# Kernel optimization log

Measured on AMD Instinct MI355X. Metric: run time of the kernel, lower is better.

Reference implementation:

```python
import jax, jax.numpy as jnp
import numpy as np

# Dim order: [N, K, C, P, Q, R, S]; memory levels: [L0_Registers, L1_Accumulator, L2_Scratchpad, L3_DRAM]
# Tensor types: 0=Input(N,C,P,Q) 1=Weight(K,C,R,S) 2=Output(N,K,P,Q)
DIM_MASK = jnp.array([[1,0,1,1,1,0,0],
                      [0,1,1,0,0,1,1],
                      [1,1,0,1,1,0,0]], dtype=bool)
# reuse dims: Input->K, Weight->N,P,Q, Output->C,R,S
REUSE_MASK = jnp.array([[0,1,0,0,0,0,0],
                        [1,0,0,1,1,0,0],
                        [0,0,1,0,0,1,1]], dtype=bool)

BYTES = 4.0
CLK_MHZ = 1000.0
DRAM_BW_GB_S = 100.0
PE_MAC_EPA_PJ = 0.56
L0_REG_EPA_PJ = 0.18
L1_BASE_EPA_PJ = 0.52
L1_COEFF_PJ_KB = 0.01
L2_BASE_EPA_PJ = 1.2
L2_COEFF_PJ_KB = 0.002
AREA_PER_PE = 0.01
AREA_PER_KB = 0.005

G = 500000  # number of (unfused) layers / fusion groups


def setup_inputs() -> dict:
    key = jax.random.key(0)
    k1, k2 = jax.random.split(key)
    temporal = 1.0 + jax.random.uniform(k1, (G, 7, 4), dtype=jnp.float32)
    spatial = 1.0 + jax.random.uniform(k2, (G, 7, 4), dtype=jnp.float32)
    return {
        "temporal_factors": temporal,
        "spatial_factors": spatial,
        "num_pes": jnp.array([256.0], dtype=jnp.float32),
        "buffer_sizes_kb": jnp.array([1.0, 64.0, 512.0], dtype=jnp.float32),  # L0, L1, L2
    }


def _masked_prod(x, mask):
    # x: [G,7,L], mask: [3,7] -> [G,3,L] product over masked dims
    return jnp.prod(jnp.where(mask[None, :, :, None], x[:, None, :, :], 1.0), axis=2)


def reference(temporal_factors, spatial_factors, num_pes, buffer_sizes_kb):
    pe = num_pes[0]
    sq = jnp.sqrt(pe)

    cumTS = jnp.cumprod(temporal_factors * spatial_factors, axis=2)  # prefix prod over levels
    cumT = jnp.cumprod(temporal_factors, axis=2)
    sufT = jnp.flip(jnp.cumprod(jnp.flip(temporal_factors, 2), 2), 2)  # suffix prod over levels

    macs = jnp.prod(cumTS[:, :, -1], axis=1)  # [G] product of full dim sizes

    fp = _masked_prod(cumTS, DIM_MASK)      # [G,3,4] data footprint up to level l
    outer = _masked_prod(sufT, DIM_MASK)    # [G,3,4] outer iterations from level l up
    ru = _masked_prod(cumT, REUSE_MASK)     # [G,3,4] reuse factor up to level l

    # interfaces (upper->lower): L3->L2, L2->L1, L1->L0
    low = jnp.array([2, 1, 0])
    up = jnp.array([3, 2, 1])
    acc = (fp[:, :, low] * (outer[:, :, up] / (ru[:, :, low] + 1e-9)) * BYTES).sum(axis=1)  # [G,3]

    # latency
    onchip_bw = 2.0 * sq * BYTES * CLK_MHZ * 1e6 / 1e9
    bw = jnp.stack([jnp.full((), DRAM_BW_GB_S), onchip_bw, onchip_bw])  # upper level bw per interface
    mem_lat = acc / (bw[None, :] * 1e9 + 1e-9)
    comp_lat = macs / (pe * CLK_MHZ * 1e6 + 1e-9)
    total_latency = jnp.maximum(comp_lat, mem_lat.max(axis=1)).sum()

    # energy (per interface, keyed by lower level: L2, L1, L0)
    epa = jnp.stack([
        L2_BASE_EPA_PJ + L2_COEFF_PJ_KB * buffer_sizes_kb[2],
        L1_BASE_EPA_PJ + L1_COEFF_PJ_KB * (buffer_sizes_kb[1] / sq),
        jnp.full((), L0_REG_EPA_PJ),
    ])
    total_energy = (macs * PE_MAC_EPA_PJ).sum() + ((acc / 4.0) @ epa).sum()

    # buffer mismatch for buffer levels L0, L1, L2
    req_kb = fp[:, :, :3].sum(axis=1) * BYTES / 1024.0  # [G,3]
    deficit = jax.nn.relu(req_kb - buffer_sizes_kb[None, :])
    total_mismatch = (deficit ** 2).sum()

    area = pe * AREA_PER_PE + (buffer_sizes_kb * AREA_PER_KB).sum()
    return (total_latency, total_energy, area, total_mismatch)
```

## Files before the change

kernel.cpp:

```cpp
#include <hip/hip_runtime.h>
#include <hip/hip_bf16.h>


typedef const __attribute__((address_space(1))) void* gptr_t;
typedef __attribute__((address_space(3))) void* lptr_t;

#define BLK 256
#define NBK 256

__global__ __launch_bounds__(BLK) void hpm_main(
    const float* __restrict__ T, const float* __restrict__ S,
    const float* __restrict__ PE, const float* __restrict__ BUF,
    double* __restrict__ part, int G)
{
    __shared__ float ldsT[2][BLK * 28];
    __shared__ float ldsS[2][BLK * 28];

    const int tid = threadIdx.x;
    const int wid = tid >> 6;
    const int NTF = G / BLK;
    const int b   = blockIdx.x;
    const int cnt = (NTF > b) ? ((NTF - 1 - b) / NBK + 1) : 0;

    const float pe = PE[0];
    const float sq = sqrtf(pe);
    const float b0 = BUF[0], b1 = BUF[1], b2 = BUF[2];
    const float bw_dram   = 100.0f * 1e9f + 1e-9f;
    const float bw_onchip = sq * 8e9f + 1e-9f;
    const float epa0 = 1.2f  + 0.002f * b2;
    const float epa1 = 0.52f + 0.01f  * (b1 / sq);
    const float epa2 = 0.18f;
    const float inv_pe = 1.0f / (pe * 1e9f + 1e-9f);

    constexpr unsigned IN_D = 0x1D, WT_D = 0x66, OU_D = 0x1B;
    constexpr unsigned IN_R = 0x02, WT_R = 0x19, OU_R = 0x64;

    auto issue = [&](int t, int buf) {
        const float* gT = T + (size_t)t * BLK * 28;
        const float* gS = S + (size_t)t * BLK * 28;
        #pragma unroll
        for (int k = 0; k < 7; ++k) {
            const int fidx = k * BLK + tid;
            const int uoff = (k * BLK + wid * 64) * 4;
            __builtin_amdgcn_global_load_lds((gptr_t)(gT + (size_t)fidx * 4),
                                             (lptr_t)&ldsT[buf][uoff], 16, 0, 0);
            __builtin_amdgcn_global_load_lds((gptr_t)(gS + (size_t)fidx * 4),
                                             (lptr_t)&ldsS[buf][uoff], 16, 0, 0);
        }
    };

    double latA = 0.0, enA = 0.0, misA = 0.0;

    auto accumulate = [&](const float4* tv, const float4* sv) {
        float fpI[3] = {1.f,1.f,1.f}, fpW[3] = {1.f,1.f,1.f}, fpO[3] = {1.f,1.f,1.f};
        float otI[3] = {1.f,1.f,1.f}, otW[3] = {1.f,1.f,1.f}, otO[3] = {1.f,1.f,1.f};
        float ruI[3] = {1.f,1.f,1.f}, ruW[3] = {1.f,1.f,1.f}, ruO[3] = {1.f,1.f,1.f};
        float macs = 1.f;

        #pragma unroll
        for (int d = 0; d < 7; ++d) {
            const float4 tt = tv[d];
            const float4 ss = sv[d];

            const float ct0 = tt.x;
            const float ct1 = ct0 * tt.y;
            const float ct2 = ct1 * tt.z;
            const float u0 = tt.x * ss.x, u1 = tt.y * ss.y;
            const float u2 = tt.z * ss.z, u3 = tt.w * ss.w;
            const float cs0 = u0;
            const float cs1 = cs0 * u1;
            const float cs2 = cs1 * u2;
            const float cs3 = cs2 * u3;
            const float st3 = tt.w;
            const float st2 = tt.z * st3;
            const float st1 = tt.y * st2;

            macs *= cs3;

            if ((IN_D >> d) & 1) {
                fpI[0] *= cs0; fpI[1] *= cs1; fpI[2] *= cs2;
                otI[0] *= st1; otI[1] *= st2; otI[2] *= st3;
            }
            if ((WT_D >> d) & 1) {
                fpW[0] *= cs0; fpW[1] *= cs1; fpW[2] *= cs2;
                otW[0] *= st1; otW[1] *= st2; otW[2] *= st3;
            }
            if ((OU_D >> d) & 1) {
                fpO[0] *= cs0; fpO[1] *= cs1; fpO[2] *= cs2;
                otO[0] *= st1; otO[1] *= st2; otO[2] *= st3;
            }
            if ((IN_R >> d) & 1) { ruI[0] *= ct0; ruI[1] *= ct1; ruI[2] *= ct2; }
            if ((WT_R >> d) & 1) { ruW[0] *= ct0; ruW[1] *= ct1; ruW[2] *= ct2; }
            if ((OU_R >> d) & 1) { ruO[0] *= ct0; ruO[1] *= ct1; ruO[2] *= ct2; }
        }

        const float acc0 = 4.f * ( fpI[2] * otI[2] / (ruI[2] + 1e-9f)
                                 + fpW[2] * otW[2] / (ruW[2] + 1e-9f)
                                 + fpO[2] * otO[2] / (ruO[2] + 1e-9f) );
        const float acc1 = 4.f * ( fpI[1] * otI[1] / (ruI[1] + 1e-9f)
                                 + fpW[1] * otW[1] / (ruW[1] + 1e-9f)
                                 + fpO[1] * otO[1] / (ruO[1] + 1e-9f) );
        const float acc2 = 4.f * ( fpI[0] * otI[0] / (ruI[0] + 1e-9f)
                                 + fpW[0] * otW[0] / (ruW[0] + 1e-9f)
                                 + fpO[0] * otO[0] / (ruO[0] + 1e-9f) );

        const float ml = fmaxf(acc0 / bw_dram, fmaxf(acc1, acc2) / bw_onchip);
        const float cl = macs * inv_pe;
        latA += (double)fmaxf(cl, ml);

        enA += (double)(macs * 0.56f + (acc0 * epa0 + acc1 * epa1 + acc2 * epa2) * 0.25f);

        const float c = 4.f / 1024.f;
        const float r0 = (fpI[0] + fpW[0] + fpO[0]) * c;
        const float r1 = (fpI[1] + fpW[1] + fpO[1]) * c;
        const float r2 = (fpI[2] + fpW[2] + fpO[2]) * c;
        const float d0 = fmaxf(r0 - b0, 0.f);
        const float d1 = fmaxf(r1 - b1, 0.f);
        const float d2 = fmaxf(r2 - b2, 0.f);
        misA += (double)d0 * d0 + (double)d1 * d1 + (double)d2 * d2;
    };

    if (cnt > 0) issue(b, 0);
    if (cnt > 1) issue(b + NBK, 1);

    for (int i = 0; i < cnt; ++i) {
        if (i + 1 < cnt) { asm volatile("s_waitcnt vmcnt(14)" ::: "memory"); }
        else             { asm volatile("s_waitcnt vmcnt(0)"  ::: "memory"); }
        __builtin_amdgcn_sched_barrier(0);
        __builtin_amdgcn_s_barrier();
        __builtin_amdgcn_sched_barrier(0);

        const int buf = i & 1;
        float4 tv[7], sv[7];
        {
            const float4* Tl = reinterpret_cast<const float4*>(&ldsT[buf][tid * 28]);
            const float4* Sl = reinterpret_cast<const float4*>(&ldsS[buf][tid * 28]);
            #pragma unroll
            for (int d = 0; d < 7; ++d) { tv[d] = Tl[d]; sv[d] = Sl[d]; }
        }
        asm volatile("s_waitcnt lgkmcnt(0)" ::: "memory");
        __builtin_amdgcn_sched_barrier(0);
        __builtin_amdgcn_s_barrier();
        __builtin_amdgcn_sched_barrier(0);

        if (i + 2 < cnt) issue(b + (size_t)(i + 2) * NBK, buf);

        accumulate(tv, sv);
    }

    if (b == 0) {
        const int g = NTF * BLK + tid;
        if (g < G) {
            float4 tv[7], sv[7];
            const float4* Tp = reinterpret_cast<const float4*>(T) + (size_t)g * 7;
            const float4* Sp = reinterpret_cast<const float4*>(S) + (size_t)g * 7;
            #pragma unroll
            for (int d = 0; d < 7; ++d) { tv[d] = Tp[d]; sv[d] = Sp[d]; }
            accumulate(tv, sv);
        }
    }

    #pragma unroll
    for (int off = 32; off > 0; off >>= 1) {
        latA += __shfl_down(latA, off);
        enA  += __shfl_down(enA,  off);
        misA += __shfl_down(misA, off);
    }

    __shared__ double sred[3][4];
    const int lane = tid & 63;
    if (lane == 0) { sred[0][wid] = latA; sred[1][wid] = enA; sred[2][wid] = misA; }
    __syncthreads();

    if (tid == 0) {
        double L = 0.0, E = 0.0, M = 0.0;
        #pragma unroll
        for (int w = 0; w < 4; ++w) { L += sred[0][w]; E += sred[1][w]; M += sred[2][w]; }
        part[0 * NBK + blockIdx.x] = L;
        part[1 * NBK + blockIdx.x] = E;
        part[2 * NBK + blockIdx.x] = M;
    }
}

__global__ __launch_bounds__(256) void hpm_final(
    const double* __restrict__ part,
    const float* __restrict__ PE, const float* __restrict__ BUF,
    float* __restrict__ out)
{
    const int tid = threadIdx.x;
    double L = 0.0, E = 0.0, M = 0.0;
    if (tid < NBK) {
        L = part[0 * NBK + tid];
        E = part[1 * NBK + tid];
        M = part[2 * NBK + tid];
    }

    #pragma unroll
    for (int off = 32; off > 0; off >>= 1) {
        L += __shfl_down(L, off);
        E += __shfl_down(E, off);
        M += __shfl_down(M, off);
    }

    __shared__ double sred[3][4];
    const int wid  = tid >> 6;
    const int lane = tid & 63;
    if (lane == 0) { sred[0][wid] = L; sred[1][wid] = E; sred[2][wid] = M; }
    __syncthreads();

    if (tid == 0) {
        double Lt = 0.0, Et = 0.0, Mt = 0.0;
        #pragma unroll
        for (int w = 0; w < 4; ++w) { Lt += sred[0][w]; Et += sred[1][w]; Mt += sred[2][w]; }
        out[0] = (float)Lt;
        out[1] = (float)Et;
        out[2] = PE[0] * 0.01f + (BUF[0] + BUF[1] + BUF[2]) * 0.005f;
        out[3] = (float)Mt;
    }
}

extern "C" void kernel_launch(void* const* d_in, const int* in_sizes, int n_in,
                              void* d_out, int out_size, void* d_ws, size_t ws_size,
                              hipStream_t stream) {
    const float* T   = (const float*)d_in[0];
    const float* S   = (const float*)d_in[1];
    const float* PE  = (const float*)d_in[2];
    const float* BUF = (const float*)d_in[3];
    float* out = (float*)d_out;
    double* ws = (double*)d_ws;

    const int G = in_sizes[0] / 28;

    hipLaunchKernelGGL(hpm_main, dim3(NBK), dim3(BLK), 0, stream,
                       T, S, PE, BUF, ws, G);
    hipLaunchKernelGGL(hpm_final, dim3(1), dim3(256), 0, stream,
                       ws, PE, BUF, out);
}
```

Before: 26.25 us.

## Give each wavefront its own LDS pipeline and replace divisions with fast reciprocals

Work is now split into 64-element tiles assigned to individual wavefronts, each with a private double-buffered LDS region, so the block-wide s_barrier calls in the streaming loop are removed. Divisions in the access computations are replaced with v_rcp_f32 and precomputed inverse bandwidths. The intent is to remove barrier stalls between waves and cut the cost of the divides. Fast reciprocal adds small rounding differences, and the tail now runs on the last wave instead of block 0.

```diff
diff --git a/kernel.cpp b/kernel.cpp
--- a/kernel.cpp
+++ b/kernel.cpp
@@ -5,47 +5,56 @@
 typedef const __attribute__((address_space(1))) void* gptr_t;
 typedef __attribute__((address_space(3))) void* lptr_t;
 
-#define BLK 256
-#define NBK 256
+#define BLK   256
+#define NBK   256
+#define WPB   4
+#define NWAVE (NBK * WPB)
+#define TGRP  64
+
+__device__ __forceinline__ float fast_rcp(float x) {
+    float r;
+    asm("v_rcp_f32 %0, %1" : "=v"(r) : "v"(x));
+    return r;
+}
 
 __global__ __launch_bounds__(BLK) void hpm_main(
     const float* __restrict__ T, const float* __restrict__ S,
     const float* __restrict__ PE, const float* __restrict__ BUF,
     double* __restrict__ part, int G)
 {
-    __shared__ float ldsT[2][BLK * 28];
-    __shared__ float ldsS[2][BLK * 28];
-
-    const int tid = threadIdx.x;
-    const int wid = tid >> 6;
-    const int NTF = G / BLK;
-    const int b   = blockIdx.x;
-    const int cnt = (NTF > b) ? ((NTF - 1 - b) / NBK + 1) : 0;
+    __shared__ float lds[WPB][2][2][TGRP * 28];
+
+    const int tid  = threadIdx.x;
+    const int w    = tid >> 6;
+    const int lane = tid & 63;
+    const int W    = blockIdx.x * WPB + w;
+    const int NT   = G / TGRP;
+    const int cnt  = (NT > W) ? ((NT - 1 - W) / NWAVE + 1) : 0;
 
     const float pe = PE[0];
     const float sq = sqrtf(pe);
     const float b0 = BUF[0], b1 = BUF[1], b2 = BUF[2];
-    const float bw_dram   = 100.0f * 1e9f + 1e-9f;
-    const float bw_onchip = sq * 8e9f + 1e-9f;
+    const float inv_bw_dram   = 1.0f / (100.0f * 1e9f + 1e-9f);
+    const float inv_bw_onchip = 1.0f / (sq * 8e9f + 1e-9f);
     const float epa0 = 1.2f  + 0.002f * b2;
     const float epa1 = 0.52f + 0.01f  * (b1 / sq);
     const float epa2 = 0.18f;
     const float inv_pe = 1.0f / (pe * 1e9f + 1e-9f);
+    asm volatile("s_waitcnt vmcnt(0) lgkmcnt(0)" ::: "memory");
 
     constexpr unsigned IN_D = 0x1D, WT_D = 0x66, OU_D = 0x1B;
     constexpr unsigned IN_R = 0x02, WT_R = 0x19, OU_R = 0x64;
 
     auto issue = [&](int t, int buf) {
-        const float* gT = T + (size_t)t * BLK * 28;
-        const float* gS = S + (size_t)t * BLK * 28;
+        const float* gT = T + (size_t)t * (TGRP * 28);
+        const float* gS = S + (size_t)t * (TGRP * 28);
         #pragma unroll
         for (int k = 0; k < 7; ++k) {
-            const int fidx = k * BLK + tid;
-            const int uoff = (k * BLK + wid * 64) * 4;
-            __builtin_amdgcn_global_load_lds((gptr_t)(gT + (size_t)fidx * 4),
-                                             (lptr_t)&ldsT[buf][uoff], 16, 0, 0);
-            __builtin_amdgcn_global_load_lds((gptr_t)(gS + (size_t)fidx * 4),
-                                             (lptr_t)&ldsS[buf][uoff], 16, 0, 0);
+            const int fo = (k * 64 + lane) * 4;
+            __builtin_amdgcn_global_load_lds((gptr_t)(gT + fo),
+                                             (lptr_t)&lds[w][buf][0][k * 256], 16, 0, 0);
+            __builtin_amdgcn_global_load_lds((gptr_t)(gS + fo),
+                                             (lptr_t)&lds[w][buf][1][k * 256], 16, 0, 0);
         }
     };
 
@@ -94,17 +103,17 @@
             if ((OU_R >> d) & 1) { ruO[0] *= ct0; ruO[1] *= ct1; ruO[2] *= ct2; }
         }
 
-        const float acc0 = 4.f * ( fpI[2] * otI[2] / (ruI[2] + 1e-9f)
-                                 + fpW[2] * otW[2] / (ruW[2] + 1e-9f)
-                                 + fpO[2] * otO[2] / (ruO[2] + 1e-9f) );
-        const float acc1 = 4.f * ( fpI[1] * otI[1] / (ruI[1] + 1e-9f)
-                                 + fpW[1] * otW[1] / (ruW[1] + 1e-9f)
-                                 + fpO[1] * otO[1] / (ruO[1] + 1e-9f) );
-        const float acc2 = 4.f * ( fpI[0] * otI[0] / (ruI[0] + 1e-9f)
-                                 + fpW[0] * otW[0] / (ruW[0] + 1e-9f)
-                                 + fpO[0] * otO[0] / (ruO[0] + 1e-9f) );
-
-        const float ml = fmaxf(acc0 / bw_dram, fmaxf(acc1, acc2) / bw_onchip);
+        const float acc0 = 4.f * ( fpI[2] * otI[2] * fast_rcp(ruI[2] + 1e-9f)
+                                 + fpW[2] * otW[2] * fast_rcp(ruW[2] + 1e-9f)
+                                 + fpO[2] * otO[2] * fast_rcp(ruO[2] + 1e-9f) );
+        const float acc1 = 4.f * ( fpI[1] * otI[1] * fast_rcp(ruI[1] + 1e-9f)
+                                 + fpW[1] * otW[1] * fast_rcp(ruW[1] + 1e-9f)
+                                 + fpO[1] * otO[1] * fast_rcp(ruO[1] + 1e-9f) );
+        const float acc2 = 4.f * ( fpI[0] * otI[0] * fast_rcp(ruI[0] + 1e-9f)
+                                 + fpW[0] * otW[0] * fast_rcp(ruW[0] + 1e-9f)
+                                 + fpO[0] * otO[0] * fast_rcp(ruO[0] + 1e-9f) );
+
+        const float ml = fmaxf(acc0 * inv_bw_dram, fmaxf(acc1, acc2) * inv_bw_onchip);
         const float cl = macs * inv_pe;
         latA += (double)fmaxf(cl, ml);
 
@@ -120,36 +129,31 @@
         misA += (double)d0 * d0 + (double)d1 * d1 + (double)d2 * d2;
     };
 
-    if (cnt > 0) issue(b, 0);
-    if (cnt > 1) issue(b + NBK, 1);
+    if (cnt > 0) issue(W, 0);
+    if (cnt > 1) issue(W + NWAVE, 1);
 
     for (int i = 0; i < cnt; ++i) {
-        if (i + 1 < cnt) { asm volatile("s_waitcnt vmcnt(14)" ::: "memory"); }
-        else             { asm volatile("s_waitcnt vmcnt(0)"  ::: "memory"); }
-        __builtin_amdgcn_sched_barrier(0);
-        __builtin_amdgcn_s_barrier();
-        __builtin_amdgcn_sched_barrier(0);
+        if (i + 1 < cnt) asm volatile("s_waitcnt vmcnt(14)" ::: "memory");
+        else             asm volatile("s_waitcnt vmcnt(0)"  ::: "memory");
 
         const int buf = i & 1;
         float4 tv[7], sv[7];
         {
-            const float4* Tl = reinterpret_cast<const float4*>(&ldsT[buf][tid * 28]);
-            const float4* Sl = reinterpret_cast<const float4*>(&ldsS[buf][tid * 28]);
+            const float4* Tl = reinterpret_cast<const float4*>(&lds[w][buf][0][lane * 28]);
+            const float4* Sl = reinterpret_cast<const float4*>(&lds[w][buf][1][lane * 28]);
             #pragma unroll
             for (int d = 0; d < 7; ++d) { tv[d] = Tl[d]; sv[d] = Sl[d]; }
         }
         asm volatile("s_waitcnt lgkmcnt(0)" ::: "memory");
         __builtin_amdgcn_sched_barrier(0);
-        __builtin_amdgcn_s_barrier();
-        __builtin_amdgcn_sched_barrier(0);
-
-        if (i + 2 < cnt) issue(b + (size_t)(i + 2) * NBK, buf);
+
+        if (i + 2 < cnt) issue(W + (i + 2) * NWAVE, buf);
 
         accumulate(tv, sv);
     }
 
-    if (b == 0) {
-        const int g = NTF * BLK + tid;
+    if (W == NWAVE - 1) {
+        const int g = NT * TGRP + lane;
         if (g < G) {
             float4 tv[7], sv[7];
             const float4* Tp = reinterpret_cast<const float4*>(T) + (size_t)g * 7;
@@ -167,15 +171,14 @@
         misA += __shfl_down(misA, off);
     }
 
-    __shared__ double sred[3][4];
-    const int lane = tid & 63;
-    if (lane == 0) { sred[0][wid] = latA; sred[1][wid] = enA; sred[2][wid] = misA; }
+    __shared__ double sred[3][WPB];
+    if (lane == 0) { sred[0][w] = latA; sred[1][w] = enA; sred[2][w] = misA; }
     __syncthreads();
 
     if (tid == 0) {
         double L = 0.0, E = 0.0, M = 0.0;
         #pragma unroll
-        for (int w = 0; w < 4; ++w) { L += sred[0][w]; E += sred[1][w]; M += sred[2][w]; }
+        for (int v = 0; v < WPB; ++v) { L += sred[0][v]; E += sred[1][v]; M += sred[2][v]; }
         part[0 * NBK + blockIdx.x] = L;
         part[1 * NBK + blockIdx.x] = E;
         part[2 * NBK + blockIdx.x] = M;
@@ -211,7 +214,7 @@
     if (tid == 0) {
         double Lt = 0.0, Et = 0.0, Mt = 0.0;
         #pragma unroll
-        for (int w = 0; w < 4; ++w) { Lt += sred[0][w]; Et += sred[1][w]; Mt += sred[2][w]; }
+        for (int v = 0; v < 4; ++v) { Lt += sred[0][v]; Et += sred[1][v]; Mt += sred[2][v]; }
         out[0] = (float)Lt;
         out[1] = (float)Et;
         out[2] = PE[0] * 0.01f + (BUF[0] + BUF[1] + BUF[2]) * 0.005f;
```

Result: no change. 25.93 us, median of 2 (-1.2%).
